# Performance work log

Measured on AMD Instinct MI355X. Metric: run time of the kernel, lower is better.

## Reference

```python
import jax, jax.numpy as jnp
import numpy as np

B = 4096
P_HID = 1024
H_HID = 512
MAX_P = 128
MAX_HE = MAX_P // 3  # 42
TAU = 1.0
EPS = 1e-20


def setup_inputs() -> dict:
    key = jax.random.key(0)
    ks = jax.random.split(key, 12)
    s_p = 1.0 / np.sqrt(P_HID)
    s_h = 1.0 / np.sqrt(H_HID)
    # gumbel noise: g = -log(-log(U))
    u_p = jax.random.uniform(ks[3], (B, MAX_P, 2), minval=EPS, maxval=1.0)
    u_h = jax.random.uniform(ks[4], (B, MAX_HE, 2), minval=EPS, maxval=1.0)
    return {
        "particle_h": jax.random.normal(ks[0], (B, P_HID), jnp.float32),
        "edge_h": jax.random.normal(ks[1], (B, H_HID), jnp.float32),
        "hyperedge_h": jax.random.normal(ks[2], (B, H_HID), jnp.float32),
        "g_p": -jnp.log(-jnp.log(u_p)),
        "g_h": -jnp.log(-jnp.log(u_h)),
        "W1_p": jax.random.normal(ks[5], (P_HID, P_HID), jnp.float32) * s_p,
        "b1_p": jnp.zeros((P_HID,), jnp.float32),
        "W2_p": jax.random.normal(ks[6], (P_HID, MAX_P), jnp.float32) * s_p,
        "b2_p": jnp.zeros((MAX_P,), jnp.float32),
        "W1_h": jax.random.normal(ks[7], (H_HID, H_HID), jnp.float32) * s_h,
        "b1_h": jnp.zeros((H_HID,), jnp.float32),
        "W2_h": jax.random.normal(ks[8], (H_HID, MAX_HE), jnp.float32) * s_h,
        "b2_h": jnp.zeros((MAX_HE,), jnp.float32),
    }


def _gumbel_hard_st(logits, g, tau):
    """F.gumbel_softmax(stack([l,-l],-1), tau, hard=True)[...,0] (straight-through)."""
    y = jax.nn.softmax((jnp.stack([logits, -logits], axis=-1) + g) / tau, axis=-1)
    y0 = y[..., 0]
    hard0 = (y0 > y[..., 1]).astype(y0.dtype)
    return hard0 + y0 - jax.lax.stop_gradient(y0)


def _mlp(x, W1, b1, W2, b2):
    return jax.nn.gelu(x @ W1 + b1, approximate=False) @ W2 + b2


def reference(particle_h, edge_h, hyperedge_h, g_p, g_h,
              W1_p, b1_p, W2_p, b2_p, W1_h, b1_h, W2_h, b2_h):
    particle_logits = _mlp(particle_h, W1_p, b1_p, W2_p, b2_p)      # [B, MAX_P]
    particle_mask = _gumbel_hard_st(particle_logits, g_p, TAU)      # [B, MAX_P]
    n_particles = particle_mask.sum(axis=-1).astype(jnp.int32)      # [B]

    # Ragged edge lists as a fixed padded buffer: all C(MAX_P,2) lexicographic
    # pairs (same order as torch.combinations); pair (i,j), i<j, is valid for
    # batch b iff j < n_particles[b].
    ii, jj = jnp.triu_indices(MAX_P, k=1)
    edge_index = jnp.stack([ii, jj]).astype(jnp.int32)              # [2, E_max]
    edge_valid = jj[None, :] < n_particles[:, None]                 # [B, E_max] bool

    hyperedge_logits = _mlp(hyperedge_h, W1_h, b1_h, W2_h, b2_h)    # [B, MAX_HE]
    hyperedge_mask = _gumbel_hard_st(hyperedge_logits, g_h, TAU)
    n_hyperedges = hyperedge_mask.sum(axis=-1).astype(jnp.int32)

    return (particle_mask, n_particles, edge_index, edge_valid,
            hyperedge_mask, n_hyperedges)
```

## Files before the change

kernel.cpp:

```cpp
#include <hip/hip_runtime.h>
#include <hip/hip_bf16.h>
#include <math.h>

typedef __bf16 bf16_t;
typedef bf16_t bf16x8 __attribute__((ext_vector_type(8)));
typedef float f32x4 __attribute__((ext_vector_type(4)));
typedef unsigned int u32;

#define B_SZ 4096
#define P_HID 1024
#define H_HID 512
#define MAX_P 128
#define MAX_HE 42
#define HE_PAD 64
#define E_MAX 8128
#define E_MAX4 2032

__device__ __forceinline__ void async_cp16(const bf16_t* g, bf16_t* l) {
    __builtin_amdgcn_global_load_lds(
        (const __attribute__((address_space(1))) u32*)g,
        (__attribute__((address_space(3))) u32*)l, 16, 0, 0);
}

__device__ __forceinline__ float gelu_exact(float v) {
    return 0.5f * v * (1.f + erff(v * 0.70710678118654752f));
}

template<int BM, int BN>
__global__ __launch_bounds__(256, 2) void gemm1_gelu(
    const bf16_t* __restrict__ Ahi, const bf16_t* __restrict__ Alo,
    const bf16_t* __restrict__ BThi, const bf16_t* __restrict__ BTlo,
    const float* __restrict__ bias,
    bf16_t* __restrict__ Chi, bf16_t* __restrict__ Clo,
    int N, int K)
{
    constexpr int MT = BM / 32;
    constexpr int NT = BN / 32;
    constexpr int OPS_A = BM / 16;
    constexpr int OPS_B = BN / 16;
    constexpr int NOPS = 2 * OPS_A + 2 * OPS_B;

    __shared__ __align__(16) bf16_t smem[(2 * BM + 2 * BN) * 32];
    bf16_t* const As0 = smem;
    bf16_t* const As1 = smem + BM * 32;
    bf16_t* const Bs0 = smem + 2 * BM * 32;
    bf16_t* const Bs1 = smem + 2 * BM * 32 + BN * 32;

    const int tid  = threadIdx.x;
    const int lane = tid & 63;
    const int wid  = tid >> 6;
    const int wm   = wid & 1;
    const int wn   = wid >> 1;
    const int bm   = blockIdx.y * BM;
    const int bn   = blockIdx.x * BN;

    const int srow = lane >> 2;
    const int scol = (lane & 3) * 8;

    f32x4 acc[MT][NT];
#pragma unroll
    for (int i = 0; i < MT; ++i)
#pragma unroll
        for (int j = 0; j < NT; ++j)
            acc[i][j] = (f32x4){0.f, 0.f, 0.f, 0.f};

    const bf16_t* const gA0 = Ahi  + (size_t)bm * K;
    const bf16_t* const gA1 = Alo  + (size_t)bm * K;
    const bf16_t* const gB0 = BThi + (size_t)bn * K;
    const bf16_t* const gB1 = BTlo + (size_t)bn * K;

    const int fr = lane & 15;
    const int fq = lane >> 4;

    for (int kt = 0; kt < K; kt += 32) {
        __syncthreads();
#pragma unroll
        for (int o = 0; o < NOPS; ++o) {
            if ((o & 3) != wid) continue;
            const bf16_t* gsrc;
            bf16_t* lbase;
            int q;
            if (o < OPS_A)                  { q = o;                     gsrc = gA0; lbase = As0; }
            else if (o < 2 * OPS_A)         { q = o - OPS_A;             gsrc = gA1; lbase = As1; }
            else if (o < 2 * OPS_A + OPS_B) { q = o - 2 * OPS_A;         gsrc = gB0; lbase = Bs0; }
            else                            { q = o - 2 * OPS_A - OPS_B; gsrc = gB1; lbase = Bs1; }
            async_cp16(gsrc + (size_t)(q * 16 + srow) * K + kt + scol,
                       lbase + q * 16 * 32);
        }
        __syncthreads();

        bf16x8 ah[MT], al[MT], bh[NT], bl[NT];
#pragma unroll
        for (int i = 0; i < MT; ++i) {
            const int row = wm * (BM / 2) + i * 16 + fr;
            ah[i] = *(const bf16x8*)(As0 + row * 32 + fq * 8);
            al[i] = *(const bf16x8*)(As1 + row * 32 + fq * 8);
        }
#pragma unroll
        for (int j = 0; j < NT; ++j) {
            const int row = wn * (BN / 2) + j * 16 + fr;
            bh[j] = *(const bf16x8*)(Bs0 + row * 32 + fq * 8);
            bl[j] = *(const bf16x8*)(Bs1 + row * 32 + fq * 8);
        }
#pragma unroll
        for (int i = 0; i < MT; ++i)
#pragma unroll
            for (int j = 0; j < NT; ++j) {
                acc[i][j] = __builtin_amdgcn_mfma_f32_16x16x32_bf16(ah[i], bh[j], acc[i][j], 0, 0, 0);
                acc[i][j] = __builtin_amdgcn_mfma_f32_16x16x32_bf16(ah[i], bl[j], acc[i][j], 0, 0, 0);
                acc[i][j] = __builtin_amdgcn_mfma_f32_16x16x32_bf16(al[i], bh[j], acc[i][j], 0, 0, 0);
            }
    }

#pragma unroll
    for (int i = 0; i < MT; ++i)
#pragma unroll
        for (int j = 0; j < NT; ++j) {
            const int col  = bn + wn * (BN / 2) + j * 16 + fr;
            const int row0 = bm + wm * (BM / 2) + i * 16 + fq * 4;
            const float bj = bias[col];
#pragma unroll
            for (int r = 0; r < 4; ++r) {
                float v = gelu_exact(acc[i][j][r] + bj);
                bf16_t h = (bf16_t)v;
                bf16_t l = (bf16_t)(v - (float)h);
                const size_t off = (size_t)(row0 + r) * N + col;
                Chi[off] = h;
                Clo[off] = l;
            }
        }
}

template<bool WNP>
__global__ __launch_bounds__(256, 2) void gemm2_mask(
    const bf16_t* __restrict__ Ahi, const bf16_t* __restrict__ Alo,
    const bf16_t* __restrict__ BThi, const bf16_t* __restrict__ BTlo,
    const float* __restrict__ bias, const float* __restrict__ g,
    float* __restrict__ out_mask, float* __restrict__ out_n,
    int* __restrict__ ws_n, int K, int NV)
{
    constexpr int BM = 64, BN = 64;
    constexpr int MT = 2, NT = 2;
    constexpr int OPS_A = 4, OPS_B = 4;
    constexpr int NOPS = 16;

    __shared__ __align__(16) bf16_t smem[(2 * BM + 2 * BN) * 32];
    bf16_t* const As0 = smem;
    bf16_t* const As1 = smem + BM * 32;
    bf16_t* const Bs0 = smem + 2 * BM * 32;
    bf16_t* const Bs1 = smem + 2 * BM * 32 + BN * 32;

    const int tid  = threadIdx.x;
    const int lane = tid & 63;
    const int wid  = tid >> 6;
    const int wm   = wid & 1;
    const int wn   = wid >> 1;
    const int bm   = blockIdx.y * BM;
    const int bn   = blockIdx.x * BN;

    const int srow = lane >> 2;
    const int scol = (lane & 3) * 8;

    f32x4 acc[MT][NT];
#pragma unroll
    for (int i = 0; i < MT; ++i)
#pragma unroll
        for (int j = 0; j < NT; ++j)
            acc[i][j] = (f32x4){0.f, 0.f, 0.f, 0.f};

    const bf16_t* const gA0 = Ahi  + (size_t)bm * K;
    const bf16_t* const gA1 = Alo  + (size_t)bm * K;
    const bf16_t* const gB0 = BThi + (size_t)bn * K;
    const bf16_t* const gB1 = BTlo + (size_t)bn * K;

    const int fr = lane & 15;
    const int fq = lane >> 4;

    for (int kt = 0; kt < K; kt += 32) {
        __syncthreads();
#pragma unroll
        for (int o = 0; o < NOPS; ++o) {
            if ((o & 3) != wid) continue;
            const bf16_t* gsrc;
            bf16_t* lbase;
            int q;
            if (o < OPS_A)                  { q = o;                     gsrc = gA0; lbase = As0; }
            else if (o < 2 * OPS_A)         { q = o - OPS_A;             gsrc = gA1; lbase = As1; }
            else if (o < 2 * OPS_A + OPS_B) { q = o - 2 * OPS_A;         gsrc = gB0; lbase = Bs0; }
            else                            { q = o - 2 * OPS_A - OPS_B; gsrc = gB1; lbase = Bs1; }
            async_cp16(gsrc + (size_t)(q * 16 + srow) * K + kt + scol,
                       lbase + q * 16 * 32);
        }
        __syncthreads();

        bf16x8 ah[MT], al[MT], bh[NT], bl[NT];
#pragma unroll
        for (int i = 0; i < MT; ++i) {
            const int row = wm * 32 + i * 16 + fr;
            ah[i] = *(const bf16x8*)(As0 + row * 32 + fq * 8);
            al[i] = *(const bf16x8*)(As1 + row * 32 + fq * 8);
        }
#pragma unroll
        for (int j = 0; j < NT; ++j) {
            const int row = wn * 32 + j * 16 + fr;
            bh[j] = *(const bf16x8*)(Bs0 + row * 32 + fq * 8);
            bl[j] = *(const bf16x8*)(Bs1 + row * 32 + fq * 8);
        }
#pragma unroll
        for (int i = 0; i < MT; ++i)
#pragma unroll
            for (int j = 0; j < NT; ++j) {
                acc[i][j] = __builtin_amdgcn_mfma_f32_16x16x32_bf16(ah[i], bh[j], acc[i][j], 0, 0, 0);
                acc[i][j] = __builtin_amdgcn_mfma_f32_16x16x32_bf16(ah[i], bl[j], acc[i][j], 0, 0, 0);
                acc[i][j] = __builtin_amdgcn_mfma_f32_16x16x32_bf16(al[i], bh[j], acc[i][j], 0, 0, 0);
            }
    }

#pragma unroll
    for (int i = 0; i < MT; ++i) {
#pragma unroll
        for (int r = 0; r < 4; ++r) {
            const int row = bm + wm * 32 + i * 16 + fq * 4 + r;
            float s = 0.f;
#pragma unroll
            for (int j = 0; j < NT; ++j) {
                const int col = bn + wn * 32 + j * 16 + fr;
                if (col < NV) {
                    const float v = acc[i][j][r] + bias[col];
                    const size_t idx = (size_t)row * NV + col;
                    const float g0 = g[2 * idx + 0];
                    const float g1 = g[2 * idx + 1];
                    const float m = ((v + g0) > (g1 - v)) ? 1.f : 0.f;
                    out_mask[idx] = m;
                    s += m;
                }
            }
            s += __shfl_xor(s, 1, 64);
            s += __shfl_xor(s, 2, 64);
            s += __shfl_xor(s, 4, 64);
            s += __shfl_xor(s, 8, 64);
            if (fr == 0) {
                atomicAdd(&out_n[row], s);
                if (WNP) atomicAdd(&ws_n[row], (int)s);
            }
        }
    }
}

struct PrepArgs {
    const float *ph, *hh, *W1p, *W2p, *W1h, *W2h;
    bf16_t *pA_hi, *pA_lo, *hA_hi, *hA_lo;
    bf16_t *W1pT_hi, *W1pT_lo, *W2pT_hi, *W2pT_lo;
    bf16_t *W1hT_hi, *W1hT_lo, *W2hT_hi, *W2hT_lo;
    float *out_ei; int *ws_jj;
    float *out_np, *out_nh; int *ws_np;
};

__device__ __forceinline__ void split4(const float* x, bf16_t* hi, bf16_t* lo, int i) {
    typedef bf16_t bf16x4 __attribute__((ext_vector_type(4)));
    float4 v = ((const float4*)x)[i];
    float vv[4] = {v.x, v.y, v.z, v.w};
    bf16x4 h, l;
#pragma unroll
    for (int r = 0; r < 4; ++r) {
        bf16_t hh = (bf16_t)vv[r];
        h[r] = hh;
        l[r] = (bf16_t)(vv[r] - (float)hh);
    }
    ((bf16x4*)hi)[i] = h;
    ((bf16x4*)lo)[i] = l;
}

__device__ __forceinline__ void tsplit(
    const float* W, bf16_t* Thi, bf16_t* Tlo, int K, int N,
    int t, int nx, float (*sh)[33], int tid)
{
    const int n0 = (t % nx) * 32, k0 = (t / nx) * 32;
    const int tx = tid & 31, ty = tid >> 5;
    for (int r = ty; r < 32; r += 8) {
        const int n = n0 + tx;
        sh[r][tx] = (n < N) ? W[(size_t)(k0 + r) * N + n] : 0.f;
    }
    __syncthreads();
    for (int r = ty; r < 32; r += 8) {
        const float x = sh[tx][r];
        bf16_t h = (bf16_t)x;
        bf16_t l = (bf16_t)(x - (float)h);
        const size_t off = (size_t)(n0 + r) * K + k0 + tx;
        Thi[off] = h;
        Tlo[off] = l;
    }
}

__device__ __forceinline__ int tri_off(int i) { return (i * (255 - i)) >> 1; }

__global__ __launch_bounds__(256) void prep_all(PrepArgs a)
{
    __shared__ float sh[32][33];
    const int bid = blockIdx.x;
    const int tid = threadIdx.x;

    if (bid < 4096) {
        split4(a.ph, a.pA_hi, a.pA_lo, bid * 256 + tid);
    } else if (bid < 6144) {
        split4(a.hh, a.hA_hi, a.hA_lo, (bid - 4096) * 256 + tid);
    } else if (bid < 7168) {
        tsplit(a.W1p, a.W1pT_hi, a.W1pT_lo, P_HID, P_HID, bid - 6144, 32, sh, tid);
    } else if (bid < 7296) {
        tsplit(a.W2p, a.W2pT_hi, a.W2pT_lo, P_HID, MAX_P, bid - 7168, 4, sh, tid);
    } else if (bid < 7552) {
        tsplit(a.W1h, a.W1hT_hi, a.W1hT_lo, H_HID, H_HID, bid - 7296, 16, sh, tid);
    } else if (bid < 7584) {
        tsplit(a.W2h, a.W2hT_hi, a.W2hT_lo, H_HID, MAX_HE, bid - 7552, 2, sh, tid);
    } else if (bid < 7616) {
        const int e = (bid - 7584) * 256 + tid;
        if (e < E_MAX) {
            int i = (int)((255.0 - sqrt(65025.0 - 8.0 * (double)e)) * 0.5);
            if (i < 0) i = 0;
            if (i > 126) i = 126;
            while (i > 0 && tri_off(i) > e) --i;
            while (i < 126 && tri_off(i + 1) <= e) ++i;
            const int j = i + 1 + (e - tri_off(i));
            a.out_ei[e] = (float)i;
            a.out_ei[E_MAX + e] = (float)j;
            a.ws_jj[e] = j;
        }
    } else {
        const int gi = (bid - 7616) * 256 + tid;
        if (gi < B_SZ) {
            a.out_np[gi] = 0.f;
            a.ws_np[gi] = 0;
        } else if (gi < 2 * B_SZ) {
            a.out_nh[gi - B_SZ] = 0.f;
        }
    }
}

__global__ __launch_bounds__(256) void edge_valid_kernel(
    const int* __restrict__ ws_jj, const int* __restrict__ ws_n,
    float* __restrict__ out, int total4)
{
    int idx = blockIdx.x * 256 + threadIdx.x;
    if (idx >= total4) return;
    int b = idx / E_MAX4;
    int q = idx - b * E_MAX4;
    int4 j4 = ((const int4*)ws_jj)[q];
    int n = ws_n[b];
    float4 v;
    v.x = (j4.x < n) ? 1.f : 0.f;
    v.y = (j4.y < n) ? 1.f : 0.f;
    v.z = (j4.z < n) ? 1.f : 0.f;
    v.w = (j4.w < n) ? 1.f : 0.f;
    ((float4*)out)[idx] = v;
}

extern "C" void kernel_launch(void* const* d_in, const int* in_sizes, int n_in,
                              void* d_out, int out_size, void* d_ws, size_t ws_size,
                              hipStream_t stream)
{
    const float* particle_h  = (const float*)d_in[0];
    const float* hyperedge_h = (const float*)d_in[2];
    const float* g_p  = (const float*)d_in[3];
    const float* g_h  = (const float*)d_in[4];
    const float* W1_p = (const float*)d_in[5];
    const float* b1_p = (const float*)d_in[6];
    const float* W2_p = (const float*)d_in[7];
    const float* b2_p = (const float*)d_in[8];
    const float* W1_h = (const float*)d_in[9];
    const float* b1_h = (const float*)d_in[10];
    const float* W2_h = (const float*)d_in[11];
    const float* b2_h = (const float*)d_in[12];

    float* out = (float*)d_out;
    float* out_pmask = out;
    float* out_np    = out_pmask + (size_t)B_SZ * MAX_P;
    float* out_ei    = out_np + B_SZ;
    float* out_ev    = out_ei + 2 * E_MAX;
    float* out_hmask = out_ev + (size_t)B_SZ * E_MAX;
    float* out_nh    = out_hmask + (size_t)B_SZ * MAX_HE;

    char* w = (char*)d_ws;
    bf16_t* pA_hi   = (bf16_t*)w;  w += (size_t)B_SZ * P_HID * 2;
    bf16_t* pA_lo   = (bf16_t*)w;  w += (size_t)B_SZ * P_HID * 2;
    bf16_t* hA_hi   = (bf16_t*)w;  w += (size_t)B_SZ * H_HID * 2;
    bf16_t* hA_lo   = (bf16_t*)w;  w += (size_t)B_SZ * H_HID * 2;
    bf16_t* hidp_hi = (bf16_t*)w;  w += (size_t)B_SZ * P_HID * 2;
    bf16_t* hidp_lo = (bf16_t*)w;  w += (size_t)B_SZ * P_HID * 2;
    bf16_t* hidh_hi = (bf16_t*)w;  w += (size_t)B_SZ * H_HID * 2;
    bf16_t* hidh_lo = (bf16_t*)w;  w += (size_t)B_SZ * H_HID * 2;
    bf16_t* W1pT_hi = (bf16_t*)w;  w += (size_t)P_HID * P_HID * 2;
    bf16_t* W1pT_lo = (bf16_t*)w;  w += (size_t)P_HID * P_HID * 2;
    bf16_t* W2pT_hi = (bf16_t*)w;  w += (size_t)MAX_P * P_HID * 2;
    bf16_t* W2pT_lo = (bf16_t*)w;  w += (size_t)MAX_P * P_HID * 2;
    bf16_t* W1hT_hi = (bf16_t*)w;  w += (size_t)H_HID * H_HID * 2;
    bf16_t* W1hT_lo = (bf16_t*)w;  w += (size_t)H_HID * H_HID * 2;
    bf16_t* W2hT_hi = (bf16_t*)w;  w += (size_t)HE_PAD * H_HID * 2;
    bf16_t* W2hT_lo = (bf16_t*)w;  w += (size_t)HE_PAD * H_HID * 2;
    int*    ws_np   = (int*)w;     w += B_SZ * 4;
    int*    ws_jj   = (int*)w;

    PrepArgs pa;
    pa.ph = particle_h; pa.hh = hyperedge_h;
    pa.W1p = W1_p; pa.W2p = W2_p; pa.W1h = W1_h; pa.W2h = W2_h;
    pa.pA_hi = pA_hi; pa.pA_lo = pA_lo; pa.hA_hi = hA_hi; pa.hA_lo = hA_lo;
    pa.W1pT_hi = W1pT_hi; pa.W1pT_lo = W1pT_lo;
    pa.W2pT_hi = W2pT_hi; pa.W2pT_lo = W2pT_lo;
    pa.W1hT_hi = W1hT_hi; pa.W1hT_lo = W1hT_lo;
    pa.W2hT_hi = W2hT_hi; pa.W2hT_lo = W2hT_lo;
    pa.out_ei = out_ei; pa.ws_jj = ws_jj;
    pa.out_np = out_np; pa.out_nh = out_nh; pa.ws_np = ws_np;
    prep_all<<<7664, 256, 0, stream>>>(pa);

    gemm1_gelu<64, 128><<<dim3(P_HID / 128, B_SZ / 64), 256, 0, stream>>>(
        pA_hi, pA_lo, W1pT_hi, W1pT_lo, b1_p, hidp_hi, hidp_lo, P_HID, P_HID);
    gemm1_gelu<64, 128><<<dim3(H_HID / 128, B_SZ / 64), 256, 0, stream>>>(
        hA_hi, hA_lo, W1hT_hi, W1hT_lo, b1_h, hidh_hi, hidh_lo, H_HID, H_HID);

    gemm2_mask<true><<<dim3(MAX_P / 64, B_SZ / 64), 256, 0, stream>>>(
        hidp_hi, hidp_lo, W2pT_hi, W2pT_lo, b2_p, g_p,
        out_pmask, out_np, ws_np, P_HID, MAX_P);
    gemm2_mask<false><<<dim3(1, B_SZ / 64), 256, 0, stream>>>(
        hidh_hi, hidh_lo, W2hT_hi, W2hT_lo, b2_h, g_h,
        out_hmask, out_nh, nullptr, H_HID, MAX_HE);

    edge_valid_kernel<<<(B_SZ * E_MAX4 + 255) / 256, 256, 0, stream>>>(
        ws_jj, ws_np, out_ev, B_SZ * E_MAX4);
}
```

Before: 312.8 us.

## Split-K second GEMMs with atomics, separate mask kernel, larger GEMM1 tiles

Both GEMMs now go through one templated kernel. The first-layer GEMMs use larger tiles: 128x128 for the particle MLP and 128x64 for the hyperedge MLP. The second-layer GEMMs use split-K over 4 chunks with float atomicAdd into bias-initialized logit buffers, which the prep kernel fills. A new mask kernel applies the Gumbel threshold and does the per-row counts with wave reductions, and the edge_valid kernel is restructured to two blocks per batch row so the divide is avoided. The aim is more parallelism in the small second GEMMs and fewer loads per FLOP in the first GEMMs. The cost is extra atomic traffic, an extra kernel launch, and nondeterministic summation order near the threshold.

```diff
diff --git a/kernel.cpp b/kernel.cpp
--- a/kernel.cpp
+++ b/kernel.cpp
@@ -4,6 +4,7 @@
 
 typedef __bf16 bf16_t;
 typedef bf16_t bf16x8 __attribute__((ext_vector_type(8)));
+typedef bf16_t bf16x4 __attribute__((ext_vector_type(4)));
 typedef float f32x4 __attribute__((ext_vector_type(4)));
 typedef unsigned int u32;
 
@@ -26,13 +27,13 @@
     return 0.5f * v * (1.f + erff(v * 0.70710678118654752f));
 }
 
-template<int BM, int BN>
-__global__ __launch_bounds__(256, 2) void gemm1_gelu(
+template<int BM, int BN, int MODE>
+__global__ __launch_bounds__(256, 2) void gemm_t(
     const bf16_t* __restrict__ Ahi, const bf16_t* __restrict__ Alo,
     const bf16_t* __restrict__ BThi, const bf16_t* __restrict__ BTlo,
     const float* __restrict__ bias,
-    bf16_t* __restrict__ Chi, bf16_t* __restrict__ Clo,
-    int N, int K)
+    bf16_t* __restrict__ Chi, bf16_t* __restrict__ Clo, float* __restrict__ Cf,
+    int N, int K, int kchunk)
 {
     constexpr int MT = BM / 32;
     constexpr int NT = BN / 32;
@@ -53,6 +54,7 @@
     const int wn   = wid >> 1;
     const int bm   = blockIdx.y * BM;
     const int bn   = blockIdx.x * BN;
+    const int k0   = blockIdx.z * kchunk;
 
     const int srow = lane >> 2;
     const int scol = (lane & 3) * 8;
@@ -72,7 +74,7 @@
     const int fr = lane & 15;
     const int fq = lane >> 4;
 
-    for (int kt = 0; kt < K; kt += 32) {
+    for (int kt = k0; kt < k0 + kchunk; kt += 32) {
         __syncthreads();
 #pragma unroll
         for (int o = 0; o < NOPS; ++o) {
@@ -118,146 +120,35 @@
         for (int j = 0; j < NT; ++j) {
             const int col  = bn + wn * (BN / 2) + j * 16 + fr;
             const int row0 = bm + wm * (BM / 2) + i * 16 + fq * 4;
-            const float bj = bias[col];
-#pragma unroll
-            for (int r = 0; r < 4; ++r) {
-                float v = gelu_exact(acc[i][j][r] + bj);
-                bf16_t h = (bf16_t)v;
-                bf16_t l = (bf16_t)(v - (float)h);
-                const size_t off = (size_t)(row0 + r) * N + col;
-                Chi[off] = h;
-                Clo[off] = l;
+            if (MODE == 0) {
+                const float bj = bias[col];
+#pragma unroll
+                for (int r = 0; r < 4; ++r) {
+                    float v = gelu_exact(acc[i][j][r] + bj);
+                    bf16_t h = (bf16_t)v;
+                    bf16_t l = (bf16_t)(v - (float)h);
+                    const size_t off = (size_t)(row0 + r) * N + col;
+                    Chi[off] = h;
+                    Clo[off] = l;
+                }
+            } else {
+#pragma unroll
+                for (int r = 0; r < 4; ++r)
+                    atomicAdd(&Cf[(size_t)(row0 + r) * N + col], acc[i][j][r]);
             }
         }
 }
 
-template<bool WNP>
-__global__ __launch_bounds__(256, 2) void gemm2_mask(
-    const bf16_t* __restrict__ Ahi, const bf16_t* __restrict__ Alo,
-    const bf16_t* __restrict__ BThi, const bf16_t* __restrict__ BTlo,
-    const float* __restrict__ bias, const float* __restrict__ g,
-    float* __restrict__ out_mask, float* __restrict__ out_n,
-    int* __restrict__ ws_n, int K, int NV)
-{
-    constexpr int BM = 64, BN = 64;
-    constexpr int MT = 2, NT = 2;
-    constexpr int OPS_A = 4, OPS_B = 4;
-    constexpr int NOPS = 16;
-
-    __shared__ __align__(16) bf16_t smem[(2 * BM + 2 * BN) * 32];
-    bf16_t* const As0 = smem;
-    bf16_t* const As1 = smem + BM * 32;
-    bf16_t* const Bs0 = smem + 2 * BM * 32;
-    bf16_t* const Bs1 = smem + 2 * BM * 32 + BN * 32;
-
-    const int tid  = threadIdx.x;
-    const int lane = tid & 63;
-    const int wid  = tid >> 6;
-    const int wm   = wid & 1;
-    const int wn   = wid >> 1;
-    const int bm   = blockIdx.y * BM;
-    const int bn   = blockIdx.x * BN;
-
-    const int srow = lane >> 2;
-    const int scol = (lane & 3) * 8;
-
-    f32x4 acc[MT][NT];
-#pragma unroll
-    for (int i = 0; i < MT; ++i)
-#pragma unroll
-        for (int j = 0; j < NT; ++j)
-            acc[i][j] = (f32x4){0.f, 0.f, 0.f, 0.f};
-
-    const bf16_t* const gA0 = Ahi  + (size_t)bm * K;
-    const bf16_t* const gA1 = Alo  + (size_t)bm * K;
-    const bf16_t* const gB0 = BThi + (size_t)bn * K;
-    const bf16_t* const gB1 = BTlo + (size_t)bn * K;
-
-    const int fr = lane & 15;
-    const int fq = lane >> 4;
-
-    for (int kt = 0; kt < K; kt += 32) {
-        __syncthreads();
-#pragma unroll
-        for (int o = 0; o < NOPS; ++o) {
-            if ((o & 3) != wid) continue;
-            const bf16_t* gsrc;
-            bf16_t* lbase;
-            int q;
-            if (o < OPS_A)                  { q = o;                     gsrc = gA0; lbase = As0; }
-            else if (o < 2 * OPS_A)         { q = o - OPS_A;             gsrc = gA1; lbase = As1; }
-            else if (o < 2 * OPS_A + OPS_B) { q = o - 2 * OPS_A;         gsrc = gB0; lbase = Bs0; }
-            else                            { q = o - 2 * OPS_A - OPS_B; gsrc = gB1; lbase = Bs1; }
-            async_cp16(gsrc + (size_t)(q * 16 + srow) * K + kt + scol,
-                       lbase + q * 16 * 32);
-        }
-        __syncthreads();
-
-        bf16x8 ah[MT], al[MT], bh[NT], bl[NT];
-#pragma unroll
-        for (int i = 0; i < MT; ++i) {
-            const int row = wm * 32 + i * 16 + fr;
-            ah[i] = *(const bf16x8*)(As0 + row * 32 + fq * 8);
-            al[i] = *(const bf16x8*)(As1 + row * 32 + fq * 8);
-        }
-#pragma unroll
-        for (int j = 0; j < NT; ++j) {
-            const int row = wn * 32 + j * 16 + fr;
-            bh[j] = *(const bf16x8*)(Bs0 + row * 32 + fq * 8);
-            bl[j] = *(const bf16x8*)(Bs1 + row * 32 + fq * 8);
-        }
-#pragma unroll
-        for (int i = 0; i < MT; ++i)
-#pragma unroll
-            for (int j = 0; j < NT; ++j) {
-                acc[i][j] = __builtin_amdgcn_mfma_f32_16x16x32_bf16(ah[i], bh[j], acc[i][j], 0, 0, 0);
-                acc[i][j] = __builtin_amdgcn_mfma_f32_16x16x32_bf16(ah[i], bl[j], acc[i][j], 0, 0, 0);
-                acc[i][j] = __builtin_amdgcn_mfma_f32_16x16x32_bf16(al[i], bh[j], acc[i][j], 0, 0, 0);
-            }
-    }
-
-#pragma unroll
-    for (int i = 0; i < MT; ++i) {
-#pragma unroll
-        for (int r = 0; r < 4; ++r) {
-            const int row = bm + wm * 32 + i * 16 + fq * 4 + r;
-            float s = 0.f;
-#pragma unroll
-            for (int j = 0; j < NT; ++j) {
-                const int col = bn + wn * 32 + j * 16 + fr;
-                if (col < NV) {
-                    const float v = acc[i][j][r] + bias[col];
-                    const size_t idx = (size_t)row * NV + col;
-                    const float g0 = g[2 * idx + 0];
-                    const float g1 = g[2 * idx + 1];
-                    const float m = ((v + g0) > (g1 - v)) ? 1.f : 0.f;
-                    out_mask[idx] = m;
-                    s += m;
-                }
-            }
-            s += __shfl_xor(s, 1, 64);
-            s += __shfl_xor(s, 2, 64);
-            s += __shfl_xor(s, 4, 64);
-            s += __shfl_xor(s, 8, 64);
-            if (fr == 0) {
-                atomicAdd(&out_n[row], s);
-                if (WNP) atomicAdd(&ws_n[row], (int)s);
-            }
-        }
-    }
-}
-
 struct PrepArgs {
-    const float *ph, *hh, *W1p, *W2p, *W1h, *W2h;
+    const float *ph, *hh, *W1p, *W2p, *W1h, *W2h, *b2p, *b2h;
     bf16_t *pA_hi, *pA_lo, *hA_hi, *hA_lo;
     bf16_t *W1pT_hi, *W1pT_lo, *W2pT_hi, *W2pT_lo;
     bf16_t *W1hT_hi, *W1hT_lo, *W2hT_hi, *W2hT_lo;
+    float *log_p, *log_h;
     float *out_ei; int *ws_jj;
-    float *out_np, *out_nh; int *ws_np;
 };
 
 __device__ __forceinline__ void split4(const float* x, bf16_t* hi, bf16_t* lo, int i) {
-    typedef bf16_t bf16x4 __attribute__((ext_vector_type(4)));
     float4 v = ((const float4*)x)[i];
     float vv[4] = {v.x, v.y, v.z, v.w};
     bf16x4 h, l;
@@ -325,33 +216,80 @@
             a.out_ei[E_MAX + e] = (float)j;
             a.ws_jj[e] = j;
         }
+    } else if (bid < 9664) {
+        const int i = (bid - 7616) * 256 + tid;
+        a.log_p[i] = a.b2p[i & (MAX_P - 1)];
     } else {
-        const int gi = (bid - 7616) * 256 + tid;
-        if (gi < B_SZ) {
-            a.out_np[gi] = 0.f;
-            a.ws_np[gi] = 0;
-        } else if (gi < 2 * B_SZ) {
-            a.out_nh[gi - B_SZ] = 0.f;
-        }
+        const int i = (bid - 9664) * 256 + tid;
+        const int c = i & (HE_PAD - 1);
+        a.log_h[i] = (c < MAX_HE) ? a.b2h[c] : 0.f;
+    }
+}
+
+__global__ __launch_bounds__(256) void mask_both(
+    const float* __restrict__ log_p, const float* __restrict__ g_p,
+    const float* __restrict__ log_h, const float* __restrict__ g_h,
+    float* __restrict__ out_pmask, float* __restrict__ out_np, int* __restrict__ ws_np,
+    float* __restrict__ out_hmask, float* __restrict__ out_nh)
+{
+    const int gw   = blockIdx.x * 4 + (threadIdx.x >> 6);
+    const int lane = threadIdx.x & 63;
+    float c = 0.f;
+    if (gw < B_SZ) {
+        const int row = gw;
+#pragma unroll
+        for (int h = 0; h < 2; ++h) {
+            const int i = lane + 64 * h;
+            const size_t idx = (size_t)row * MAX_P + i;
+            const float l  = log_p[idx];
+            const float g0 = g_p[2 * idx + 0];
+            const float g1 = g_p[2 * idx + 1];
+            const float m = ((l + g0) > (g1 - l)) ? 1.f : 0.f;
+            out_pmask[idx] = m;
+            c += m;
+        }
+#pragma unroll
+        for (int off = 32; off > 0; off >>= 1) c += __shfl_xor(c, off, 64);
+        if (lane == 0) { out_np[row] = c; ws_np[row] = (int)c; }
+    } else {
+        const int row = gw - B_SZ;
+        if (lane < MAX_HE) {
+            const size_t idx = (size_t)row * MAX_HE + lane;
+            const float l  = log_h[(size_t)row * HE_PAD + lane];
+            const float g0 = g_h[2 * idx + 0];
+            const float g1 = g_h[2 * idx + 1];
+            const float m = ((l + g0) > (g1 - l)) ? 1.f : 0.f;
+            out_hmask[idx] = m;
+            c = m;
+        }
+#pragma unroll
+        for (int off = 32; off > 0; off >>= 1) c += __shfl_xor(c, off, 64);
+        if (lane == 0) out_nh[row] = c;
     }
 }
 
 __global__ __launch_bounds__(256) void edge_valid_kernel(
     const int* __restrict__ ws_jj, const int* __restrict__ ws_n,
-    float* __restrict__ out, int total4)
-{
-    int idx = blockIdx.x * 256 + threadIdx.x;
-    if (idx >= total4) return;
-    int b = idx / E_MAX4;
-    int q = idx - b * E_MAX4;
-    int4 j4 = ((const int4*)ws_jj)[q];
-    int n = ws_n[b];
-    float4 v;
-    v.x = (j4.x < n) ? 1.f : 0.f;
-    v.y = (j4.y < n) ? 1.f : 0.f;
-    v.z = (j4.z < n) ? 1.f : 0.f;
-    v.w = (j4.w < n) ? 1.f : 0.f;
-    ((float4*)out)[idx] = v;
+    float* __restrict__ out)
+{
+    const int b   = blockIdx.x >> 1;
+    const int seg = blockIdx.x & 1;
+    const int n   = ws_n[b];
+    const int base = seg * (E_MAX4 / 2);
+    float* const orow = out + (size_t)b * E_MAX;
+#pragma unroll
+    for (int it = 0; it < 4; ++it) {
+        const int q = base + it * 256 + threadIdx.x;
+        if (q < base + E_MAX4 / 2) {
+            const int4 j4 = ((const int4*)ws_jj)[q];
+            float4 v;
+            v.x = (j4.x < n) ? 1.f : 0.f;
+            v.y = (j4.y < n) ? 1.f : 0.f;
+            v.z = (j4.z < n) ? 1.f : 0.f;
+            v.w = (j4.w < n) ? 1.f : 0.f;
+            ((float4*)orow)[q] = v;
+        }
+    }
 }
 
 extern "C" void kernel_launch(void* const* d_in, const int* in_sizes, int n_in,
@@ -396,33 +334,40 @@
     bf16_t* W1hT_lo = (bf16_t*)w;  w += (size_t)H_HID * H_HID * 2;
     bf16_t* W2hT_hi = (bf16_t*)w;  w += (size_t)HE_PAD * H_HID * 2;
     bf16_t* W2hT_lo = (bf16_t*)w;  w += (size_t)HE_PAD * H_HID * 2;
+    float*  log_p   = (float*)w;   w += (size_t)B_SZ * MAX_P * 4;
+    float*  log_h   = (float*)w;   w += (size_t)B_SZ * HE_PAD * 4;
     int*    ws_np   = (int*)w;     w += B_SZ * 4;
     int*    ws_jj   = (int*)w;
 
     PrepArgs pa;
     pa.ph = particle_h; pa.hh = hyperedge_h;
     pa.W1p = W1_p; pa.W2p = W2_p; pa.W1h = W1_h; pa.W2h = W2_h;
+    pa.b2p = b2_p; pa.b2h = b2_h;
     pa.pA_hi = pA_hi; pa.pA_lo = pA_lo; pa.hA_hi = hA_hi; pa.hA_lo = hA_lo;
     pa.W1pT_hi = W1pT_hi; pa.W1pT_lo = W1pT_lo;
     pa.W2pT_hi = W2pT_hi; pa.W2pT_lo = W2pT_lo;
     pa.W1hT_hi = W1hT_hi; pa.W1hT_lo = W1hT_lo;
     pa.W2hT_hi = W2hT_hi; pa.W2hT_lo = W2hT_lo;
+    pa.log_p = log_p; pa.log_h = log_h;
     pa.out_ei = out_ei; pa.ws_jj = ws_jj;
-    pa.out_np = out_np; pa.out_nh = out_nh; pa.ws_np = ws_np;
-    prep_all<<<7664, 256, 0, stream>>>(pa);
-
-    gemm1_gelu<64, 128><<<dim3(P_HID / 128, B_SZ / 64), 256, 0, stream>>>(
-        pA_hi, pA_lo, W1pT_hi, W1pT_lo, b1_p, hidp_hi, hidp_lo, P_HID, P_HID);
-    gemm1_gelu<64, 128><<<dim3(H_HID / 128, B_SZ / 64), 256, 0, stream>>>(
-        hA_hi, hA_lo, W1hT_hi, W1hT_lo, b1_h, hidh_hi, hidh_lo, H_HID, H_HID);
-
-    gemm2_mask<true><<<dim3(MAX_P / 64, B_SZ / 64), 256, 0, stream>>>(
-        hidp_hi, hidp_lo, W2pT_hi, W2pT_lo, b2_p, g_p,
-        out_pmask, out_np, ws_np, P_HID, MAX_P);
-    gemm2_mask<false><<<dim3(1, B_SZ / 64), 256, 0, stream>>>(
-        hidh_hi, hidh_lo, W2hT_hi, W2hT_lo, b2_h, g_h,
-        out_hmask, out_nh, nullptr, H_HID, MAX_HE);
-
-    edge_valid_kernel<<<(B_SZ * E_MAX4 + 255) / 256, 256, 0, stream>>>(
-        ws_jj, ws_np, out_ev, B_SZ * E_MAX4);
-}
+    prep_all<<<10688, 256, 0, stream>>>(pa);
+
+    gemm_t<128, 128, 0><<<dim3(P_HID / 128, B_SZ / 128), 256, 0, stream>>>(
+        pA_hi, pA_lo, W1pT_hi, W1pT_lo, b1_p, hidp_hi, hidp_lo, nullptr,
+        P_HID, P_HID, P_HID);
+    gemm_t<128, 64, 0><<<dim3(H_HID / 64, B_SZ / 128), 256, 0, stream>>>(
+        hA_hi, hA_lo, W1hT_hi, W1hT_lo, b1_h, hidh_hi, hidh_lo, nullptr,
+        H_HID, H_HID, H_HID);
+
+    gemm_t<128, 128, 1><<<dim3(1, B_SZ / 128, 4), 256, 0, stream>>>(
+        hidp_hi, hidp_lo, W2pT_hi, W2pT_lo, nullptr, nullptr, nullptr, log_p,
+        MAX_P, P_HID, P_HID / 4);
+    gemm_t<128, 64, 1><<<dim3(1, B_SZ / 128, 4), 256, 0, stream>>>(
+        hidh_hi, hidh_lo, W2hT_hi, W2hT_lo, nullptr, nullptr, nullptr, log_h,
+        HE_PAD, H_HID, H_HID / 4);
+
+    mask_both<<<2 * B_SZ / 4, 256, 0, stream>>>(
+        log_p, g_p, log_h, g_h, out_pmask, out_np, ws_np, out_hmask, out_nh);
+
+    edge_valid_kernel<<<2 * B_SZ, 256, 0, stream>>>(ws_jj, ws_np, out_ev);
+}
```

Result: no change. 316.8 us (+1.3%).
